# Kernel optimization log

Measured on AMD Instinct MI355X. Metric: run time of the kernel, lower is better.

The kernel has to match this reference:

```python
import jax, jax.numpy as jnp
import numpy as np

C = 256
LN_EPS = 1e-5

def setup_inputs() -> dict:
    key = jax.random.key(0)
    ks = jax.random.split(key, 12)
    B, M, N = 8, 4096, 4096
    scale = 1.0 / np.sqrt(C)
    inp = {
        'x': jax.random.normal(ks[0], (B, M, C), jnp.float32),
        'y': jax.random.normal(ks[1], (B, N, C), jnp.float32),
        'Wq': jax.random.normal(ks[2], (C, C), jnp.float32) * scale,
        'bq': jnp.zeros((C,), jnp.float32),
        'Wk': jax.random.normal(ks[3], (C, C), jnp.float32) * scale,
        'bk': jnp.zeros((C,), jnp.float32),
        'Wv': jax.random.normal(ks[4], (C, C), jnp.float32) * scale,
        'bv': jnp.zeros((C,), jnp.float32),
        'Wo': jax.random.normal(ks[5], (C, C), jnp.float32) * (scale * 1e-5),
        'bo': jnp.zeros((C,), jnp.float32),
        'gamma': jnp.ones((C,), jnp.float32),
        'beta': jnp.zeros((C,), jnp.float32),
    }
    return inp

def reference(x, y, Wq, bq, Wk, bk, Wv, bv, Wo, bo, gamma, beta):
    # projections (torch Linear: x @ W.T + b)
    q = x @ Wq.T + bq                      # [B,M,C]
    k = y @ Wk.T + bk                      # [B,N,C]
    v = y @ Wv.T + bv                      # [B,N,C]
    # scaled dot-product attention with explicit score matrix
    w = jnp.einsum('bmc,bnc->bmn', q, k) * (C ** -0.5)  # [B,M,N]
    w = jax.nn.softmax(w, axis=-1)
    h = jnp.einsum('bmn,bnc->bmc', w, v)   # [B,M,C]
    h = h @ Wo.T + bo
    z = x + h
    # LayerNorm over last dim
    mu = jnp.mean(z, axis=-1, keepdims=True)
    var = jnp.var(z, axis=-1, keepdims=True)
    out = (z - mu) * jax.lax.rsqrt(var + LN_EPS) * gamma + beta
    return out
```

## Files before the change

kernel.cpp:

```cpp
#include <hip/hip_runtime.h>
#include <hip/hip_bf16.h>

#define C_DIM 256
#define QSCALE 0.09016844f
#define WO_SCALE 1048576.0f
#define WO_INV   9.5367431640625e-07f

typedef __attribute__((ext_vector_type(8))) short bf16x8;
typedef __attribute__((ext_vector_type(4))) float f32x4;
typedef __attribute__((ext_vector_type(16))) float f32x16;

__device__ __forceinline__ void gload16(const unsigned char* g, unsigned char* l) {
    __builtin_amdgcn_global_load_lds(
        (const __attribute__((address_space(1))) void*)g,
        (__attribute__((address_space(3))) void*)l, 16, 0, 0);
}

__global__ void cvt_w_kernel(const float* __restrict__ w0, const float* __restrict__ w1,
                             const float* __restrict__ w2, const float* __restrict__ w3,
                             unsigned char* __restrict__ o0, unsigned char* __restrict__ o1,
                             unsigned char* __restrict__ o2, unsigned char* __restrict__ o3) {
    int i = (blockIdx.x * 256 + threadIdx.x) * 4;
    #pragma unroll
    for (int wsel = 0; wsel < 4; ++wsel) {
        const float* w = wsel == 0 ? w0 : (wsel == 1 ? w1 : (wsel == 2 ? w2 : w3));
        unsigned char* o = wsel == 0 ? o0 : (wsel == 1 ? o1 : (wsel == 2 ? o2 : o3));
        const float sc = (wsel == 3) ? WO_SCALE : 1.0f;
        float4 v = *reinterpret_cast<const float4*>(w + i);
        unsigned p = __builtin_amdgcn_cvt_pk_fp8_f32(v.x * sc, v.y * sc, 0, false);
        p = __builtin_amdgcn_cvt_pk_fp8_f32(v.z * sc, v.w * sc, p, true);
        *reinterpret_cast<unsigned*>(o + i) = p;
    }
}

__global__ __launch_bounds__(256, 1)
void proj_kernel(const float* __restrict__ x, const float* __restrict__ y,
                 const unsigned char* __restrict__ wq8, const unsigned char* __restrict__ wk8,
                 const unsigned char* __restrict__ wv8,
                 const float* __restrict__ bqp, const float* __restrict__ bkp,
                 const float* __restrict__ bvp,
                 unsigned char* __restrict__ qo, unsigned char* __restrict__ ko,
                 unsigned char* __restrict__ vo)
{
    __shared__ __align__(16) unsigned char ldsW[65536];
    __shared__ __align__(16) unsigned char ldsA[32768];

    const int which = blockIdx.x >> 8;
    const int tile = blockIdx.x & 255;
    const float* in = (which == 0) ? x : y;
    const unsigned char* wsrc = (which == 0) ? wq8 : (which == 1 ? wk8 : wv8);
    const float* bias = (which == 0) ? bqp : (which == 1 ? bkp : bvp);
    unsigned char* out = (which == 0) ? qo : (which == 1 ? ko : vo);
    const float oscale = (which == 0) ? QSCALE : 1.0f;

    const int tid = threadIdx.x;
    const int rowbase = tile * 128;

    #pragma unroll
    for (int it = 0; it < 16; ++it) {
        int G = it * 256 + tid;
        int c = G >> 4, p = G & 15;
        gload16(wsrc + c * 256 + ((p ^ (c & 15)) << 4), ldsW + G * 16);
    }
    #pragma unroll
    for (int it = 0; it < 32; ++it) {
        int e = it * 1024 + tid * 4;
        int r = e >> 8, c4 = e & 255;
        float4 v = *reinterpret_cast<const float4*>(in + (size_t)(rowbase + r) * C_DIM + c4);
        unsigned p = __builtin_amdgcn_cvt_pk_fp8_f32(v.x, v.y, 0, false);
        p = __builtin_amdgcn_cvt_pk_fp8_f32(v.z, v.w, p, true);
        int g = (c4 >> 4) ^ (r & 15);
        *reinterpret_cast<unsigned*>(ldsA + r * 256 + g * 16 + (c4 & 12)) = p;
    }
    __syncthreads();

    const int lane = tid & 63, wave = tid >> 6;
    const int lrow = lane & 15, lkq = lane >> 4;
    const int koff = (lkq & 1) << 3;
    const int kg = lkq >> 1;

    #pragma unroll
    for (int ms = 0; ms < 2; ++ms) {
        const int arow = wave * 32 + ms * 16 + lrow;
        long a[8];
        #pragma unroll
        for (int ks = 0; ks < 8; ++ks)
            a[ks] = *reinterpret_cast<const long*>(
                ldsA + arow * 256 + (((ks * 2 + kg) ^ (arow & 15)) << 4) + koff);

        f32x4 acc[16];
        #pragma unroll
        for (int nf = 0; nf < 16; ++nf) acc[nf] = f32x4{0.f, 0.f, 0.f, 0.f};

        #pragma unroll
        for (int nf = 0; nf < 16; ++nf) {
            const int c = nf * 16 + lrow;
            const unsigned char* wb = ldsW + c * 256;
            const int cx = c & 15;
            #pragma unroll
            for (int ks = 0; ks < 8; ++ks) {
                long b = *reinterpret_cast<const long*>(wb + (((ks * 2 + kg) ^ cx) << 4) + koff);
                acc[nf] = __builtin_amdgcn_mfma_f32_16x16x32_fp8_fp8(a[ks], b, acc[nf], 0, 0, 0);
            }
        }

        const int base = rowbase + wave * 32 + ms * 16 + lkq * 4;
        if (which != 2) {
            const int rsw = (which == 1) ? (base & 8) : 0;
            #pragma unroll
            for (int nf = 0; nf < 16; ++nf) {
                float bv = bias[nf * 16 + lrow];
                float v0 = (acc[nf][0] + bv) * oscale, v1 = (acc[nf][1] + bv) * oscale;
                float v2 = (acc[nf][2] + bv) * oscale, v3 = (acc[nf][3] + bv) * oscale;
                unsigned p = __builtin_amdgcn_cvt_pk_fp8_f32(v0, v1, 0, false);
                p = __builtin_amdgcn_cvt_pk_fp8_f32(v2, v3, p, true);
                int col = (nf * 16 + lrow) ^ rsw;
                unsigned char* o = out + (size_t)base * C_DIM + col;
                o[0]   = (unsigned char)p;
                o[256] = (unsigned char)(p >> 8);
                o[512] = (unsigned char)(p >> 16);
                o[768] = (unsigned char)(p >> 24);
            }
        } else {
            int bb = base >> 12, n0 = base & 4095;
            #pragma unroll
            for (int nf = 0; nf < 16; ++nf) {
                float bv = bias[nf * 16 + lrow];
                float v0 = acc[nf][0] + bv, v1 = acc[nf][1] + bv;
                float v2 = acc[nf][2] + bv, v3 = acc[nf][3] + bv;
                unsigned p = __builtin_amdgcn_cvt_pk_fp8_f32(v0, v1, 0, false);
                p = __builtin_amdgcn_cvt_pk_fp8_f32(v2, v3, p, true);
                int c = nf * 16 + lrow;
                *reinterpret_cast<unsigned*>(vo + ((size_t)bb * C_DIM + c) * 4096 + (n0 ^ (c & 8))) = p;
            }
        }
    }
}

__global__ __launch_bounds__(512, 1)
void attn_kernel(const unsigned char* __restrict__ qg, const unsigned char* __restrict__ kg,
                 const unsigned char* __restrict__ vtg, unsigned short* __restrict__ hg)
{
    __shared__ __align__(16) unsigned char smb[98304];

    const int tid = threadIdx.x;
    const int lane = tid & 63;
    const int w = tid >> 6;
    const int wq = w & 3;
    const int half = w >> 2;
    const int l31 = lane & 31;
    const int hi5 = lane >> 5;
    const int ksw = l31 & 15;
    const int hsw = ((l31 >> 3) & 1) << 3;
    const int vsw = ((l31 >> 2) & 1);

    const int batch = blockIdx.x & 7;
    const int mt = blockIdx.x >> 3;
    const size_t q0 = (size_t)batch * 4096 + mt * 128 + wq * 32;

    const unsigned char* kbase = kg + ((size_t)batch * 4096 + half * 2048) * 256;
    const unsigned char* vbase = vtg + (size_t)batch * 256 * 4096 + half * 2048;

    long qf[16];
    #pragma unroll
    for (int ks = 0; ks < 16; ++ks)
        qf[ks] = *reinterpret_cast<const long*>(qg + (q0 + l31) * 256 + ks * 16 + hi5 * 8);

    f32x16 o[8];
    #pragma unroll
    for (int cb = 0; cb < 8; ++cb) {
        #pragma unroll
        for (int r = 0; r < 16; ++r) o[cb][r] = 0.f;
    }

    float m_run = -__builtin_inff();
    float lsum = 0.f;

    auto stage = [&](int kb, int vb, int kt) {
        const int kv0 = kt * 32;
        unsigned char* lk = smb + (half * 2 + kb) * 8192;
        unsigned char* lv = smb + 32768 + (half * 3 + vb) * 8192;
        #pragma unroll
        for (int i = 0; i < 2; ++i) {
            int g = wq * 128 + i * 64 + lane;
            int row = g >> 4, pos = g & 15;
            gload16(kbase + (size_t)(kv0 + row) * 256 + ((pos ^ (row & 15)) << 4), lk + g * 16);
        }
        #pragma unroll
        for (int i = 0; i < 2; ++i) {
            int s = wq * 128 + i * 64 + lane;
            int c = s >> 1;
            int k2 = (s & 1) ^ ((s >> 3) & 1);
            gload16(vbase + (size_t)c * 4096 + kv0 + k2 * 16, lv + s * 16);
        }
    };

    auto do_S = [&](int kb, f32x16& sreg) {
        const unsigned char* krow = smb + (half * 2 + kb) * 8192 + l31 * 256 + ((hi5 * 8) ^ hsw);
        #pragma unroll
        for (int r = 0; r < 16; ++r) sreg[r] = 0.f;
        __builtin_amdgcn_s_setprio(1);
        #pragma unroll
        for (int ks = 0; ks < 16; ++ks) {
            long a0 = *reinterpret_cast<const long*>(krow + ((ks ^ ksw) << 4));
            sreg = __builtin_amdgcn_mfma_f32_32x32x16_fp8_fp8(a0, qf[ks], sreg, 0, 0, 0);
        }
        __builtin_amdgcn_s_setprio(0);
    };

    auto do_S_PV = [&](int kb, f32x16& sreg, long pb0, long pb1, int vb) {
        const unsigned char* krow = smb + (half * 2 + kb) * 8192 + l31 * 256 + ((hi5 * 8) ^ hsw);
        const unsigned char* vrow = smb + 32768 + (half * 3 + vb) * 8192
                                    + l31 * 32 + ((hi5 * 8) ^ hsw);
        #pragma unroll
        for (int r = 0; r < 16; ++r) sreg[r] = 0.f;
        __builtin_amdgcn_s_setprio(1);
        #pragma unroll
        for (int i = 0; i < 16; ++i) {
            long a0 = *reinterpret_cast<const long*>(krow + ((i ^ ksw) << 4));
            sreg = __builtin_amdgcn_mfma_f32_32x32x16_fp8_fp8(a0, qf[i], sreg, 0, 0, 0);
            const int ksv = i >> 3, cb = i & 7;
            long vf = *reinterpret_cast<const long*>(vrow + cb * 1024 + (((ksv ^ vsw)) << 4));
            o[cb] = __builtin_amdgcn_mfma_f32_32x32x16_fp8_fp8(
                vf, ksv ? pb1 : pb0, o[cb], 0, 0, 0);
        }
        __builtin_amdgcn_s_setprio(0);
    };

    auto do_PV = [&](long pb0, long pb1, int vb) {
        const unsigned char* vrow = smb + 32768 + (half * 3 + vb) * 8192
                                    + l31 * 32 + ((hi5 * 8) ^ hsw);
        __builtin_amdgcn_s_setprio(1);
        #pragma unroll
        for (int ksv = 0; ksv < 2; ++ksv) {
            const int k2s = (ksv ^ vsw) << 4;
            #pragma unroll
            for (int cb = 0; cb < 8; ++cb) {
                long vf = *reinterpret_cast<const long*>(vrow + cb * 1024 + k2s);
                o[cb] = __builtin_amdgcn_mfma_f32_32x32x16_fp8_fp8(
                    vf, ksv ? pb1 : pb0, o[cb], 0, 0, 0);
            }
        }
        __builtin_amdgcn_s_setprio(0);
    };

    auto do_SM = [&](f32x16& sreg, long& pb0, long& pb1) {
        float mloc = sreg[0];
        #pragma unroll
        for (int r = 1; r < 16; ++r) mloc = fmaxf(mloc, sreg[r]);
        mloc = fmaxf(mloc, __shfl_xor(mloc, 32, 64));

        if (__any(mloc > m_run + 8.0f)) {
            float mn = fmaxf(m_run, mloc);
            float al = exp2f(m_run - mn);
            m_run = mn;
            lsum *= al;
            #pragma unroll
            for (int cb = 0; cb < 8; ++cb) {
                #pragma unroll
                for (int r = 0; r < 16; ++r) o[cb][r] *= al;
            }
        }

        float ts = 0.f;
        #pragma unroll
        for (int r = 0; r < 16; ++r) { sreg[r] = exp2f(sreg[r] - m_run); ts += sreg[r]; }
        ts += __shfl_xor(ts, 32, 64);
        lsum += ts;

        unsigned Wu[4];
        #pragma unroll
        for (int a = 0; a < 4; ++a) {
            unsigned p = __builtin_amdgcn_cvt_pk_fp8_f32(sreg[4 * a], sreg[4 * a + 1], 0, false);
            Wu[a] = __builtin_amdgcn_cvt_pk_fp8_f32(sreg[4 * a + 2], sreg[4 * a + 3], p, true);
        }

        const bool h = (hi5 != 0);
        #pragma unroll
        for (int ksv = 0; ksv < 2; ++ksv) {
            unsigned snd = h ? Wu[2 * ksv] : Wu[2 * ksv + 1];
            unsigned rcv = __shfl_xor(snd, 32, 64);
            unsigned wlo = h ? rcv : Wu[2 * ksv];
            unsigned whi = h ? Wu[2 * ksv + 1] : rcv;
            long pb = (long)(((unsigned long long)whi << 32) | (unsigned long long)wlo);
            if (ksv == 0) pb0 = pb; else pb1 = pb;
        }
    };

    stage(0, 0, 0);
    __syncthreads();

    f32x16 s0;
    long pb0 = 0, pb1 = 0;

    stage(1, 1, 1);
    do_S(0, s0);
    do_SM(s0, pb0, pb1);
    __syncthreads();

    int vprv = 0, vcur = 1, vnxt = 2;
    for (int kt = 1; kt < 64; ++kt) {
        if (kt < 63) stage((kt + 1) & 1, vnxt, kt + 1);
        do_S_PV(kt & 1, s0, pb0, pb1, vprv);
        do_SM(s0, pb0, pb1);
        __syncthreads();
        vprv = vcur; vcur = vnxt; vnxt = (vnxt == 2) ? 0 : vnxt + 1;
    }
    do_PV(pb0, pb1, vprv);

    __syncthreads();

    unsigned short* pub = (unsigned short*)smb;
    float* ml = (float*)(smb + 90112);

    if (half == 1) {
        if (hi5 == 0) {
            ml[(wq * 32 + l31) * 2]     = m_run;
            ml[(wq * 32 + l31) * 2 + 1] = lsum;
        }
        unsigned short* prow = pub + (wq * 32 + l31) * 256;
        const int cxor = (l31 & 15) << 2;
        #pragma unroll
        for (int cb = 0; cb < 8; ++cb) {
            #pragma unroll
            for (int rp = 0; rp < 8; ++rp) {
                const int r = 2 * rp;
                unsigned wpk;
                float lo = o[cb][r], hi_ = o[cb][r + 1];
                asm("v_cvt_pk_bf16_f32 %0, %1, %2" : "=v"(wpk) : "v"(lo), "v"(hi_));
                int c = cb * 32 + (r & 3) + 8 * (r >> 2) + 4 * hi5;
                *reinterpret_cast<unsigned*>(prow + (c ^ cxor)) = wpk;
            }
        }
    }
    __syncthreads();

    if (half == 0) {
        float m1 = ml[(wq * 32 + l31) * 2];
        float l1 = ml[(wq * 32 + l31) * 2 + 1];
        float mm = fmaxf(m_run, m1);
        float a0 = exp2f(m_run - mm), a1 = exp2f(m1 - mm);
        float lt = lsum * a0 + l1 * a1;
        float rinv = 1.0f / lt;
        float f0 = a0 * rinv, f1 = a1 * rinv;

        const unsigned short* prow = pub + (wq * 32 + l31) * 256;
        const int cxor = (l31 & 15) << 2;
        unsigned short* tr = (unsigned short*)(smb + 65536 + wq * 4608);
        #pragma unroll
        for (int cc = 0; cc < 4; ++cc) {
            #pragma unroll
            for (int cbh = 0; cbh < 2; ++cbh) {
                const int cb = cc * 2 + cbh;
                #pragma unroll
                for (int rp = 0; rp < 8; ++rp) {
                    const int r = 2 * rp;
                    int c = cb * 32 + (r & 3) + 8 * (r >> 2) + 4 * hi5;
                    unsigned pk = *reinterpret_cast<const unsigned*>(prow + (c ^ cxor));
                    union { unsigned u; float f; } b0, b1;
                    b0.u = pk << 16; b1.u = pk & 0xffff0000u;
                    float v_lo = o[cb][r]     * f0 + b0.f * f1;
                    float v_hi = o[cb][r + 1] * f0 + b1.f * f1;
                    unsigned wpk;
                    asm("v_cvt_pk_bf16_f32 %0, %1, %2" : "=v"(wpk) : "v"(v_lo), "v"(v_hi));
                    int c_local = 32 * cbh + (r & 3) + 8 * (r >> 2) + 4 * hi5;
                    *reinterpret_cast<unsigned*>(tr + l31 * 72 + c_local) = wpk;
                }
            }
            __builtin_amdgcn_s_waitcnt(0);
            #pragma unroll
            for (int i = 0; i < 4; ++i) {
                int idx = i * 64 + lane;
                int q = idx >> 3, ch = idx & 7;
                uint4 d = *reinterpret_cast<const uint4*>(tr + q * 72 + ch * 8);
                *reinterpret_cast<uint4*>(hg + (q0 + q) * 256 + cc * 64 + ch * 8) = d;
            }
        }
    }
}

__global__ __launch_bounds__(256, 1)
void out_kernel(const unsigned short* __restrict__ hb, const unsigned char* __restrict__ wo8,
                const float* __restrict__ bo, const float* __restrict__ xg,
                const float* __restrict__ gamma, const float* __restrict__ beta,
                float* __restrict__ outg)
{
    __shared__ __align__(16) unsigned char ldsW[65536];
    __shared__ __align__(16) unsigned char ldsA[32768];

    const int tid = threadIdx.x;
    const int rowbase = blockIdx.x * 128;

    #pragma unroll
    for (int it = 0; it < 16; ++it) {
        int G = it * 256 + tid;
        int c = G >> 4, p = G & 15;
        gload16(wo8 + c * 256 + ((p ^ (c & 15)) << 4), ldsW + G * 16);
    }
    #pragma unroll
    for (int it = 0; it < 16; ++it) {
        int e = it * 2048 + tid * 8;
        int r = e >> 8, c8 = e & 255;
        uint4 d = *reinterpret_cast<const uint4*>(hb + (size_t)(rowbase + r) * C_DIM + c8);
        union { unsigned u; float f; } f0, f1, f2, f3, f4, f5, f6, f7;
        f0.u = d.x << 16; f1.u = d.x & 0xffff0000u;
        f2.u = d.y << 16; f3.u = d.y & 0xffff0000u;
        f4.u = d.z << 16; f5.u = d.z & 0xffff0000u;
        f6.u = d.w << 16; f7.u = d.w & 0xffff0000u;
        unsigned p0 = __builtin_amdgcn_cvt_pk_fp8_f32(f0.f, f1.f, 0, false);
        p0 = __builtin_amdgcn_cvt_pk_fp8_f32(f2.f, f3.f, p0, true);
        unsigned p1 = __builtin_amdgcn_cvt_pk_fp8_f32(f4.f, f5.f, 0, false);
        p1 = __builtin_amdgcn_cvt_pk_fp8_f32(f6.f, f7.f, p1, true);
        int g = (c8 >> 4) ^ (r & 15);
        uint2 pk; pk.x = p0; pk.y = p1;
        *reinterpret_cast<uint2*>(ldsA + r * 256 + g * 16 + (c8 & 8)) = pk;
    }
    __syncthreads();

    const int lane = tid & 63, wave = tid >> 6;
    const int lrow = lane & 15, lkq = lane >> 4;
    const int koff = (lkq & 1) << 3;
    const int kg = lkq >> 1;

    #pragma unroll
    for (int ms = 0; ms < 2; ++ms) {
        const int arow = wave * 32 + ms * 16 + lrow;
        long a[8];
        #pragma unroll
        for (int ks = 0; ks < 8; ++ks)
            a[ks] = *reinterpret_cast<const long*>(
                ldsA + arow * 256 + (((ks * 2 + kg) ^ (arow & 15)) << 4) + koff);

        f32x4 acc[16];
        #pragma unroll
        for (int nf = 0; nf < 16; ++nf) acc[nf] = f32x4{0.f, 0.f, 0.f, 0.f};

        #pragma unroll
        for (int nf = 0; nf < 16; ++nf) {
            const int c = nf * 16 + lrow;
            const unsigned char* wb = ldsW + c * 256;
            const int cx = c & 15;
            #pragma unroll
            for (int ks = 0; ks < 8; ++ks) {
                long b = *reinterpret_cast<const long*>(wb + (((ks * 2 + kg) ^ cx) << 4) + koff);
                acc[nf] = __builtin_amdgcn_mfma_f32_16x16x32_fp8_fp8(a[ks], b, acc[nf], 0, 0, 0);
            }
        }

        const int base = rowbase + wave * 32 + ms * 16 + lkq * 4;

        #pragma unroll
        for (int nf = 0; nf < 16; ++nf) {
            float bv = bo[nf * 16 + lrow];
            #pragma unroll
            for (int r = 0; r < 4; ++r) {
                size_t row = base + r;
                acc[nf][r] = acc[nf][r] * WO_INV + bv + xg[row * C_DIM + nf * 16 + lrow];
            }
        }

        float mu[4], rstd[4];
        #pragma unroll
        for (int r = 0; r < 4; ++r) {
            float s1 = 0.f, s2 = 0.f;
            #pragma unroll
            for (int nf = 0; nf < 16; ++nf) { float v = acc[nf][r]; s1 += v; s2 += v * v; }
            #pragma unroll
            for (int off = 1; off < 16; off <<= 1) {
                s1 += __shfl_xor(s1, off, 64);
                s2 += __shfl_xor(s2, off, 64);
            }
            float m = s1 * (1.f / 256.f);
            mu[r] = m;
            rstd[r] = rsqrtf(s2 * (1.f / 256.f) - m * m + 1e-5f);
        }

        #pragma unroll
        for (int nf = 0; nf < 16; ++nf) {
            float g = gamma[nf * 16 + lrow];
            float bt = beta[nf * 16 + lrow];
            #pragma unroll
            for (int r = 0; r < 4; ++r) {
                size_t row = base + r;
                outg[row * C_DIM + nf * 16 + lrow] = (acc[nf][r] - mu[r]) * rstd[r] * g + bt;
            }
        }
    }
}

extern "C" void kernel_launch(void* const* d_in, const int* in_sizes, int n_in,
                              void* d_out, int out_size, void* d_ws, size_t ws_size,
                              hipStream_t stream) {
    const float* x     = (const float*)d_in[0];
    const float* y     = (const float*)d_in[1];
    const float* Wq    = (const float*)d_in[2];
    const float* bq    = (const float*)d_in[3];
    const float* Wk    = (const float*)d_in[4];
    const float* bk    = (const float*)d_in[5];
    const float* Wv    = (const float*)d_in[6];
    const float* bv    = (const float*)d_in[7];
    const float* Wo    = (const float*)d_in[8];
    const float* bo    = (const float*)d_in[9];
    const float* gamma = (const float*)d_in[10];
    const float* beta  = (const float*)d_in[11];
    float* out = (float*)d_out;

    unsigned char* ws = (unsigned char*)d_ws;
    unsigned char* wq8 = ws;
    unsigned char* wk8 = ws + 65536;
    unsigned char* wv8 = ws + 131072;
    unsigned char* wo8 = ws + 196608;
    unsigned char* q_b = ws + 262144;
    unsigned char* k_b = q_b + 8388608;
    unsigned char* v_b = k_b + 8388608;
    unsigned short* h_b = (unsigned short*)(v_b + 8388608);

    cvt_w_kernel<<<64, 256, 0, stream>>>(Wq, Wk, Wv, Wo, wq8, wk8, wv8, wo8);

    proj_kernel<<<768, 256, 0, stream>>>(x, y, wq8, wk8, wv8, bq, bk, bv, q_b, k_b, v_b);

    attn_kernel<<<256, 512, 0, stream>>>(q_b, k_b, v_b, h_b);

    out_kernel<<<256, 256, 0, stream>>>(h_b, wo8, bo, x, gamma, beta, out);
}
```

Baseline: 187.3 us.

## Stage 64-key K/V tiles and run S, softmax, PV sequentially per subtile

Each stage now loads two 32-key K/V subtiles into double-buffered LDS, which grows the shared buffer to 128 KB and halves the number of block barriers. The old three-buffer V rotation and the fused do_S_PV loop are removed. Each subtile now runs QK^T, then softmax, then PV in turn. This trims barrier and staging overhead, but gives up the interleaving of the current tile's QK^T MFMAs with the previous tile's PV MFMAs, so softmax latency may be less hidden.

```diff
diff --git a/kernel.cpp b/kernel.cpp
--- a/kernel.cpp
+++ b/kernel.cpp
@@ -141,7 +141,7 @@
 void attn_kernel(const unsigned char* __restrict__ qg, const unsigned char* __restrict__ kg,
                  const unsigned char* __restrict__ vtg, unsigned short* __restrict__ hg)
 {
-    __shared__ __align__(16) unsigned char smb[98304];
+    __shared__ __align__(16) unsigned char smb[131072];
 
     const int tid = threadIdx.x;
     const int lane = tid & 63;
@@ -176,27 +176,31 @@
     float m_run = -__builtin_inff();
     float lsum = 0.f;
 
-    auto stage = [&](int kb, int vb, int kt) {
-        const int kv0 = kt * 32;
-        unsigned char* lk = smb + (half * 2 + kb) * 8192;
-        unsigned char* lv = smb + 32768 + (half * 3 + vb) * 8192;
-        #pragma unroll
-        for (int i = 0; i < 2; ++i) {
-            int g = wq * 128 + i * 64 + lane;
-            int row = g >> 4, pos = g & 15;
-            gload16(kbase + (size_t)(kv0 + row) * 256 + ((pos ^ (row & 15)) << 4), lk + g * 16);
-        }
-        #pragma unroll
-        for (int i = 0; i < 2; ++i) {
-            int s = wq * 128 + i * 64 + lane;
-            int c = s >> 1;
-            int k2 = (s & 1) ^ ((s >> 3) & 1);
-            gload16(vbase + (size_t)c * 4096 + kv0 + k2 * 16, lv + s * 16);
+    auto stage = [&](int buf, int rt) {
+        const int kv0 = rt * 64;
+        #pragma unroll
+        for (int sub = 0; sub < 2; ++sub) {
+            unsigned char* lk = smb + (half * 4 + buf * 2 + sub) * 8192;
+            unsigned char* lv = smb + 65536 + (half * 4 + buf * 2 + sub) * 8192;
+            #pragma unroll
+            for (int i = 0; i < 2; ++i) {
+                int g = wq * 128 + i * 64 + lane;
+                int row = g >> 4, pos = g & 15;
+                gload16(kbase + (size_t)(kv0 + sub * 32 + row) * 256 + ((pos ^ (row & 15)) << 4),
+                        lk + g * 16);
+            }
+            #pragma unroll
+            for (int i = 0; i < 2; ++i) {
+                int s = wq * 128 + i * 64 + lane;
+                int c = s >> 1;
+                int k2 = (s & 1) ^ ((s >> 3) & 1);
+                gload16(vbase + (size_t)c * 4096 + kv0 + sub * 32 + k2 * 16, lv + s * 16);
+            }
         }
     };
 
-    auto do_S = [&](int kb, f32x16& sreg) {
-        const unsigned char* krow = smb + (half * 2 + kb) * 8192 + l31 * 256 + ((hi5 * 8) ^ hsw);
+    auto do_S = [&](int kidx, f32x16& sreg) {
+        const unsigned char* krow = smb + kidx * 8192 + l31 * 256 + ((hi5 * 8) ^ hsw);
         #pragma unroll
         for (int r = 0; r < 16; ++r) sreg[r] = 0.f;
         __builtin_amdgcn_s_setprio(1);
@@ -204,42 +208,6 @@
         for (int ks = 0; ks < 16; ++ks) {
             long a0 = *reinterpret_cast<const long*>(krow + ((ks ^ ksw) << 4));
             sreg = __builtin_amdgcn_mfma_f32_32x32x16_fp8_fp8(a0, qf[ks], sreg, 0, 0, 0);
-        }
-        __builtin_amdgcn_s_setprio(0);
-    };
-
-    auto do_S_PV = [&](int kb, f32x16& sreg, long pb0, long pb1, int vb) {
-        const unsigned char* krow = smb + (half * 2 + kb) * 8192 + l31 * 256 + ((hi5 * 8) ^ hsw);
-        const unsigned char* vrow = smb + 32768 + (half * 3 + vb) * 8192
-                                    + l31 * 32 + ((hi5 * 8) ^ hsw);
-        #pragma unroll
-        for (int r = 0; r < 16; ++r) sreg[r] = 0.f;
-        __builtin_amdgcn_s_setprio(1);
-        #pragma unroll
-        for (int i = 0; i < 16; ++i) {
-            long a0 = *reinterpret_cast<const long*>(krow + ((i ^ ksw) << 4));
-            sreg = __builtin_amdgcn_mfma_f32_32x32x16_fp8_fp8(a0, qf[i], sreg, 0, 0, 0);
-            const int ksv = i >> 3, cb = i & 7;
-            long vf = *reinterpret_cast<const long*>(vrow + cb * 1024 + (((ksv ^ vsw)) << 4));
-            o[cb] = __builtin_amdgcn_mfma_f32_32x32x16_fp8_fp8(
-                vf, ksv ? pb1 : pb0, o[cb], 0, 0, 0);
-        }
-        __builtin_amdgcn_s_setprio(0);
-    };
-
-    auto do_PV = [&](long pb0, long pb1, int vb) {
-        const unsigned char* vrow = smb + 32768 + (half * 3 + vb) * 8192
-                                    + l31 * 32 + ((hi5 * 8) ^ hsw);
-        __builtin_amdgcn_s_setprio(1);
-        #pragma unroll
-        for (int ksv = 0; ksv < 2; ++ksv) {
-            const int k2s = (ksv ^ vsw) << 4;
-            #pragma unroll
-            for (int cb = 0; cb < 8; ++cb) {
-                long vf = *reinterpret_cast<const long*>(vrow + cb * 1024 + k2s);
-                o[cb] = __builtin_amdgcn_mfma_f32_32x32x16_fp8_fp8(
-                    vf, ksv ? pb1 : pb0, o[cb], 0, 0, 0);
-            }
         }
         __builtin_amdgcn_s_setprio(0);
     };
@@ -287,28 +255,43 @@
         }
     };
 
-    stage(0, 0, 0);
+    auto do_PV = [&](long pb0, long pb1, int vidx) {
+        const unsigned char* vrow = smb + 65536 + vidx * 8192 + l31 * 32 + ((hi5 * 8) ^ hsw);
+        __builtin_amdgcn_s_setprio(1);
+        #pragma unroll
+        for (int ksv = 0; ksv < 2; ++ksv) {
+            const int k2s = (ksv ^ vsw) << 4;
+            #pragma unroll
+            for (int cb = 0; cb < 8; ++cb) {
+                long vf = *reinterpret_cast<const long*>(vrow + cb * 1024 + k2s);
+                o[cb] = __builtin_amdgcn_mfma_f32_32x32x16_fp8_fp8(
+                    vf, ksv ? pb1 : pb0, o[cb], 0, 0, 0);
+            }
+        }
+        __builtin_amdgcn_s_setprio(0);
+    };
+
+    stage(0, 0);
     __syncthreads();
 
     f32x16 s0;
     long pb0 = 0, pb1 = 0;
 
-    stage(1, 1, 1);
-    do_S(0, s0);
-    do_SM(s0, pb0, pb1);
-    __syncthreads();
-
-    int vprv = 0, vcur = 1, vnxt = 2;
-    for (int kt = 1; kt < 64; ++kt) {
-        if (kt < 63) stage((kt + 1) & 1, vnxt, kt + 1);
-        do_S_PV(kt & 1, s0, pb0, pb1, vprv);
+    for (int rt = 0; rt < 32; ++rt) {
+        const int cur = rt & 1;
+        if (rt < 31) stage(cur ^ 1, rt + 1);
+        const int b0 = half * 4 + cur * 2;
+
+        do_S(b0, s0);
         do_SM(s0, pb0, pb1);
+        do_PV(pb0, pb1, b0);
+
+        do_S(b0 + 1, s0);
+        do_SM(s0, pb0, pb1);
+        do_PV(pb0, pb1, b0 + 1);
+
         __syncthreads();
-        vprv = vcur; vcur = vnxt; vnxt = (vnxt == 2) ? 0 : vnxt + 1;
-    }
-    do_PV(pb0, pb1, vprv);
-
-    __syncthreads();
+    }
 
     unsigned short* pub = (unsigned short*)smb;
     float* ml = (float*)(smb + 90112);
@@ -357,10 +340,10 @@
                     const int r = 2 * rp;
                     int c = cb * 32 + (r & 3) + 8 * (r >> 2) + 4 * hi5;
                     unsigned pk = *reinterpret_cast<const unsigned*>(prow + (c ^ cxor));
-                    union { unsigned u; float f; } b0, b1;
-                    b0.u = pk << 16; b1.u = pk & 0xffff0000u;
-                    float v_lo = o[cb][r]     * f0 + b0.f * f1;
-                    float v_hi = o[cb][r + 1] * f0 + b1.f * f1;
+                    union { unsigned u; float f; } b0u, b1u;
+                    b0u.u = pk << 16; b1u.u = pk & 0xffff0000u;
+                    float v_lo = o[cb][r]     * f0 + b0u.f * f1;
+                    float v_hi = o[cb][r + 1] * f0 + b1u.f * f1;
                     unsigned wpk;
                     asm("v_cvt_pk_bf16_f32 %0, %1, %2" : "=v"(wpk) : "v"(v_lo), "v"(v_hi));
                     int c_local = 32 * cbh + (r & 3) + 8 * (r >> 2) + 4 * hi5;
```

After: 189.5 us. No clear change (+1.2%).
